# Kernel tuning notes

Hardware: AMD Instinct MI355X
Metric: run time of the kernel (lower is better)

## Reference

```python
import jax, jax.numpy as jnp
import numpy as np

B, LQ, LK, H = 16, 8192, 128, 128  # note LK == H is required by the final matmul
SCALE = float(np.sqrt(H))


def setup_inputs() -> dict:
    key = jax.random.key(0)
    k1, k2, k3, k4, k5, k6 = jax.random.split(key, 6)
    x1 = jax.random.normal(k1, (B, LQ, H), dtype=jnp.float32)
    x2 = jax.random.normal(k2, (B, LK, H), dtype=jnp.float32)
    x3 = jax.random.randint(k3, (B, LQ, LK), 0, 2).astype(bool)
    bound = 1.0 / np.sqrt(H)  # torch Linear default init
    wq = jax.random.uniform(k4, (H, H), minval=-bound, maxval=bound, dtype=jnp.float32)
    wk = jax.random.uniform(k5, (H, H), minval=-bound, maxval=bound, dtype=jnp.float32)
    wv = jax.random.uniform(k6, (H, H), minval=-bound, maxval=bound, dtype=jnp.float32)
    return {"x1": x1, "x2": x2, "x3": x3, "wq": wq, "wk": wk, "wv": wv}


def reference(x1, x2, x3, wq, wk, wv):
    q = x1 @ wq.T                                   # (B, Lq, H)
    k = x2 @ wk.T                                   # (B, Lk, H)
    qk = jnp.einsum('bqh,bkh->bqk', q, k) / SCALE   # (B, Lq, Lk)
    qk = jnp.where(x3, -jnp.inf, qk)                # masked_fill_ where mask is True
    attn_weight = jax.nn.softmax(qk, axis=-1)       # softmax over Lk
    v = x2 @ wv.T                                   # (B, Lk, H)
    # v @ attn_weight^T: contracts v's H axis with attn_weight's Lk axis (H == Lk)
    attn = jnp.matmul(v, jnp.swapaxes(attn_weight, -2, -1))  # (B, Lk, Lq)
    return attn
```

## Files before the change

kernel.cpp:

```cpp
#include <hip/hip_runtime.h>
#include <hip/hip_bf16.h>
#include <stdint.h>

typedef __bf16 bf16_t;
typedef __bf16 bf16x8 __attribute__((ext_vector_type(8)));
typedef float  f32x4  __attribute__((ext_vector_type(4)));
typedef float  f32x16 __attribute__((ext_vector_type(16)));
typedef unsigned int uint;
typedef uint uintx4 __attribute__((ext_vector_type(4)));

#define MFMA16(a,b,c) __builtin_amdgcn_mfma_f32_16x16x32_bf16((a),(b),(c),0,0,0)
#define MFMA32(a,b,c) __builtin_amdgcn_mfma_f32_32x32x16_bf16((a),(b),(c),0,0,0)

constexpr int NB = 16;
constexpr int LQ = 8192;
constexpr int LK = 128;
constexpr int H  = 128;

constexpr float C1 = 1.4426950408889634f / 11.313708498984761f;

constexpr size_t WS_FLAG = 0;
constexpr size_t WS_MV   = 1024;

__device__ __forceinline__ unsigned swz(unsigned row, unsigned byte) {
  return row * 256u + (byte ^ ((row & 15u) << 4));
}

__device__ __forceinline__ bf16x8 cvt_frag(const float* p) {
  f32x4 u0 = *(const f32x4*)p;
  f32x4 u1 = *(const f32x4*)(p + 4);
  bf16x8 v;
  #pragma unroll
  for (int e = 0; e < 4; ++e) { v[e] = (bf16_t)u0[e]; v[e + 4] = (bf16_t)u1[e]; }
  return v;
}

__device__ __forceinline__ f32x16 zero16() {
  f32x16 z;
  #pragma unroll
  for (int i = 0; i < 16; ++i) z[i] = 0.f;
  return z;
}

__device__ __forceinline__ uint pkbf(float a, float b) {
  uint d;
  asm("v_cvt_pk_bf16_f32 %0, %1, %2" : "=v"(d) : "v"(a), "v"(b));
  return d;
}

__device__ __forceinline__ void gl16(const void* g, void* l) {
  __builtin_amdgcn_global_load_lds(
      (const __attribute__((address_space(1))) uint32_t*)g,
      (__attribute__((address_space(3))) uint32_t*)l, 16, 0, 0);
}

__global__ __launch_bounds__(512) void prep_kernel(
    const float* __restrict__ x2, const float* __restrict__ wq,
    const float* __restrict__ wk, const float* __restrict__ wv,
    const unsigned* __restrict__ x3w, uint8_t* __restrict__ ws)
{
  __shared__ uint8_t sP[131072];
  __shared__ int sF32, sBig;
  const int tid = threadIdx.x;
  const int b = blockIdx.x >> 1, which = blockIdx.x & 1;
  const int l = tid & 63, w = tid >> 6, q31 = l & 31, hi2 = l >> 5;
  uint8_t* sOut = sP + 98304;

  if (which == 0) {
    if (blockIdx.x == 0) {
      if (tid == 0) { sF32 = 0; sBig = 0; }
      __syncthreads();
      int f = 0, g = 0;
      #pragma unroll
      for (int j = 0; j < 4; ++j) {
        unsigned v = x3w[tid * 4 + j];
        if (v == 0x3f800000u) f = 1;
        else if (v > 1u) g = 1;
      }
      if (f) sF32 = 1;
      if (g) sBig = 1;
      __syncthreads();
      if (tid == 0) *(int*)(ws + WS_FLAG) = (sF32 == 0 && sBig == 1) ? 1 : 0;
    }

    {
      const int row = tid >> 2, c0 = (tid & 3) * 32;
      #pragma unroll
      for (int wh = 0; wh < 2; ++wh) {
        const float* W = wh ? wk : wq;
        uint8_t* dst = sP + wh * 32768;
        const float* s = W + row * H + c0;
        #pragma unroll
        for (int j = 0; j < 32; ++j)
          *(bf16_t*)(dst + swz(c0 + j, row * 2)) = (bf16_t)s[j];
      }
    }
    __syncthreads();

    {
      const int lo = l & 15, hi = l >> 4;
      bf16x8 a4[4];
      #pragma unroll
      for (int kk = 0; kk < 4; ++kk)
        a4[kk] = *(const bf16x8*)(sP + swz(16 * w + lo, kk * 64 + hi * 16));
      bf16_t* W2T = (bf16_t*)(sP + 65536);
      #pragma unroll
      for (int t = 0; t < 8; ++t) {
        f32x4 c = {0.f, 0.f, 0.f, 0.f};
        #pragma unroll
        for (int kk = 0; kk < 4; ++kk)
          c = MFMA16(a4[kk], *(const bf16x8*)(sP + 32768 + swz(16 * t + lo, kk * 64 + hi * 16)), c);
        #pragma unroll
        for (int r = 0; r < 4; ++r)
          W2T[(16 * w + hi * 4 + r) * H + 16 * t + lo] = (bf16_t)c[r];
      }
    }
    __syncthreads();

    if (w < 4) {
      const int wb = w;
      bf16x8 axf[8];
      const float* x2r = x2 + ((size_t)b * LK + 32 * wb + q31) * H;
      #pragma unroll
      for (int kt = 0; kt < 8; ++kt)
        axf[kt] = cvt_frag(x2r + kt * 16 + 8 * hi2);
      const bf16_t* W2Tl = (const bf16_t*)(sP + 65536);
      #pragma unroll
      for (int nt = 0; nt < 4; ++nt) {
        f32x16 c = zero16();
        #pragma unroll
        for (int kt = 0; kt < 8; ++kt)
          c = MFMA32(axf[kt],
                     *(const bf16x8*)(W2Tl + (size_t)(nt * 32 + q31) * H + kt * 16 + 8 * hi2), c);
        #pragma unroll
        for (int r = 0; r < 16; ++r)
          *(bf16_t*)(sOut + swz(32 * wb + (r & 3) + 8 * (r >> 2) + 4 * hi2,
                                (nt * 32 + q31) * 2)) = (bf16_t)c[r];
      }
    }
  } else {
    if (w < 4) {
      const int wb = w;
      bf16x8 axf[8];
      const float* x2r = x2 + ((size_t)b * LK + 32 * wb + q31) * H;
      #pragma unroll
      for (int kt = 0; kt < 8; ++kt)
        axf[kt] = cvt_frag(x2r + kt * 16 + 8 * hi2);
      #pragma unroll
      for (int nt = 0; nt < 4; ++nt) {
        f32x16 c = zero16();
        #pragma unroll
        for (int kt = 0; kt < 8; ++kt)
          c = MFMA32(axf[kt],
                     cvt_frag(wv + (size_t)(nt * 32 + q31) * H + kt * 16 + 8 * hi2), c);
        #pragma unroll
        for (int r = 0; r < 16; ++r)
          *(bf16_t*)(sOut + swz(32 * wb + (r & 3) + 8 * (r >> 2) + 4 * hi2,
                                (nt * 32 + q31) * 2)) = (bf16_t)c[r];
      }
    }
  }
  __syncthreads();

  {
    const uint4* src = (const uint4*)sOut;
    uint4* dst = (uint4*)(ws + WS_MV + (size_t)b * 65536 + (size_t)which * 32768);
    #pragma unroll
    for (int j = 0; j < 4; ++j)
      dst[tid + j * 512] = src[tid + j * 512];
  }
}


#define CONV_S_PB(XR, MU, QROW)                                                \
  {                                                                            \
    bf16x8 xbf[8];                                                             \
    _Pragma("unroll")                                                          \
    for (int kt = 0; kt < 8; ++kt) {                                           \
      _Pragma("unroll")                                                        \
      for (int e = 0; e < 4; ++e) {                                            \
        xbf[kt][e]     = (bf16_t)XR[2 * kt][e];                                \
        xbf[kt][e + 4] = (bf16_t)XR[2 * kt + 1][e];                            \
      }                                                                        \
    }                                                                          \
    const uint* mrowW = (const uint*)x3 + (QROW) * LK;                         \
    _Pragma("unroll")                                                          \
    for (int half = 0; half < 2; ++half) {                                     \
      const int jt0 = half * 2, jt1 = half * 2 + 1;                            \
      f32x16 s0 = zero16(), s1 = zero16();                                     \
      __builtin_amdgcn_s_setprio(1);                                           \
      _Pragma("unroll")                                                        \
      for (int kt = 0; kt < 8; ++kt) {                                         \
        s0 = MFMA32(*(const bf16x8*)(sM + swz(jt0 * 32 + q31, kt * 32 + hi2 * 16)), \
                    xbf[kt], s0);                                              \
        s1 = MFMA32(*(const bf16x8*)(sM + swz(jt1 * 32 + q31, kt * 32 + hi2 * 16)), \
                    xbf[kt], s1);                                              \
      }                                                                        \
      __builtin_amdgcn_s_setprio(0);                                           \
      _Pragma("unroll")                                                        \
      for (int jj = 0; jj < 2; ++jj) {                                         \
        f32x16& sj = jj ? s1 : s0;                                             \
        const int jt = half * 2 + jj;                                          \
        _Pragma("unroll")                                                      \
        for (int rg = 0; rg < 4; ++rg) {                                       \
          uint m0, m1, m2, m3;                                                 \
          if (byteMode) {                                                      \
            uint u = MU[jt * 4 + rg];                                          \
            m0 = u & 0xffu; m1 = (u >> 8) & 0xffu;                             \
            m2 = (u >> 16) & 0xffu; m3 = u >> 24;                              \
          } else {                                                             \
            uint4 mw = *(const uint4*)(mrowW + jt * 32 + 8 * rg + 4 * hi2);    \
            m0 = mw.x; m1 = mw.y; m2 = mw.z; m3 = mw.w;                        \
          }                                                                    \
          float p0 = __builtin_amdgcn_exp2f(sj[rg * 4 + 0] * C1);              \
          float p1 = __builtin_amdgcn_exp2f(sj[rg * 4 + 1] * C1);              \
          float p2 = __builtin_amdgcn_exp2f(sj[rg * 4 + 2] * C1);              \
          float p3 = __builtin_amdgcn_exp2f(sj[rg * 4 + 3] * C1);              \
          sj[rg * 4 + 0] = m0 ? 0.f : p0;                                      \
          sj[rg * 4 + 1] = m1 ? 0.f : p1;                                      \
          sj[rg * 4 + 2] = m2 ? 0.f : p2;                                      \
          sj[rg * 4 + 3] = m3 ? 0.f : p3;                                      \
        }                                                                      \
        _Pragma("unroll")                                                      \
        for (int h = 0; h < 2; ++h) {                                          \
          uint A = pkbf(sj[h * 8 + 0], sj[h * 8 + 1]);                         \
          uint C = pkbf(sj[h * 8 + 2], sj[h * 8 + 3]);                         \
          uint B = pkbf(sj[h * 8 + 4], sj[h * 8 + 5]);                         \
          uint D = pkbf(sj[h * 8 + 6], sj[h * 8 + 7]);                         \
          asm("v_permlane32_swap_b32 %0, %1" : "+v"(A), "+v"(B));              \
          asm("v_permlane32_swap_b32 %0, %1" : "+v"(C), "+v"(D));              \
          uintx4 t2; t2.x = A; t2.y = C; t2.z = B; t2.w = D;                   \
          pb[jt * 2 + h] = __builtin_bit_cast(bf16x8, t2);                     \
        }                                                                      \
      }                                                                        \
    }                                                                          \
  }

#define O_STORE(Q0W)                                                           \
  {                                                                            \
    f32x16 dacc = zero16();                                                    \
    {                                                                          \
      f32x16 o0 = zero16(), o1 = zero16();                                     \
      __builtin_amdgcn_s_setprio(1);                                           \
      _Pragma("unroll")                                                        \
      for (int kt = 0; kt < 8; ++kt) {                                         \
        dacc = MFMA32(ones1, pb[kt], dacc);                                    \
        o0 = MFMA32(*(const bf16x8*)(sV + swz(0 * 32 + q31, kt * 32 + hi2 * 16)), pb[kt], o0); \
        o1 = MFMA32(*(const bf16x8*)(sV + swz(1 * 32 + q31, kt * 32 + hi2 * 16)), pb[kt], o1); \
      }                                                                        \
      __builtin_amdgcn_s_setprio(0);                                           \
      const float inv = 1.0f / dacc[0];                                        \
      _Pragma("unroll")                                                        \
      for (int r = 0; r < 16; ++r) {                                           \
        const int ibase = (r & 3) + 8 * (r >> 2) + 4 * hi2;                    \
        __builtin_nontemporal_store(o0[r] * inv,                               \
            &out[((size_t)b * LK + ibase) * LQ + (Q0W) + q31]);                \
        __builtin_nontemporal_store(o1[r] * inv,                               \
            &out[((size_t)b * LK + 32 + ibase) * LQ + (Q0W) + q31]);           \
      }                                                                        \
      f32x16 o2 = zero16(), o3 = zero16();                                     \
      __builtin_amdgcn_s_setprio(1);                                           \
      _Pragma("unroll")                                                        \
      for (int kt = 0; kt < 8; ++kt) {                                         \
        o2 = MFMA32(*(const bf16x8*)(sV + swz(2 * 32 + q31, kt * 32 + hi2 * 16)), pb[kt], o2); \
        o3 = MFMA32(*(const bf16x8*)(sV + swz(3 * 32 + q31, kt * 32 + hi2 * 16)), pb[kt], o3); \
      }                                                                        \
      __builtin_amdgcn_s_setprio(0);                                           \
      _Pragma("unroll")                                                        \
      for (int r = 0; r < 16; ++r) {                                           \
        const int ibase = (r & 3) + 8 * (r >> 2) + 4 * hi2;                    \
        __builtin_nontemporal_store(o2[r] * inv,                               \
            &out[((size_t)b * LK + 64 + ibase) * LQ + (Q0W) + q31]);           \
        __builtin_nontemporal_store(o3[r] * inv,                               \
            &out[((size_t)b * LK + 96 + ibase) * LQ + (Q0W) + q31]);           \
      }                                                                        \
    }                                                                          \
  }

__global__ __launch_bounds__(256, 2) void attn_kernel(
    const float* __restrict__ x1, const void* __restrict__ x3,
    const uint8_t* __restrict__ ws, float* __restrict__ out)
{
  __shared__ uint8_t sm[65536];
  uint8_t* sM = sm;
  uint8_t* sV = sm + 32768;

  const int tid = threadIdx.x, blk = blockIdx.x;
  const int xcd = blk & 7;
  const int t   = blk >> 3;
  const int b   = ((t & 1) << 3) | xcd;
  const int qc  = (t >> 1) * 256;
  const int l = tid & 63, w4 = tid >> 6;
  const int q31 = l & 31, hi2 = l >> 5;
  const int byteMode = *(const int*)(ws + WS_FLAG);

  const int q0w0 = qc + w4 * 64;
  const int q0w1 = q0w0 + 32;
  const size_t qrow0 = (size_t)b * LQ + q0w0 + q31;
  const size_t qrow1 = qrow0 + 32;

  {
    const uint8_t* g = ws + WS_MV + (size_t)b * 65536;
    #pragma unroll
    for (int j = 0; j < 16; ++j)
      gl16(g + tid * 16 + j * 4096, sm + tid * 16 + j * 4096);
  }

  f32x4 xr0[16];
  uint mu0[16];
  {
    const float* xp = x1 + qrow0 * H;
    #pragma unroll
    for (int kt = 0; kt < 8; ++kt) {
      xr0[2 * kt]     = *(const f32x4*)(xp + kt * 16 + 8 * hi2);
      xr0[2 * kt + 1] = *(const f32x4*)(xp + kt * 16 + 8 * hi2 + 4);
    }
    if (byteMode) {
      const uint8_t* mp = (const uint8_t*)x3 + qrow0 * LK;
      #pragma unroll
      for (int jt = 0; jt < 4; ++jt)
        #pragma unroll
        for (int rg = 0; rg < 4; ++rg)
          mu0[jt * 4 + rg] = *(const uint*)(mp + jt * 32 + 8 * rg + 4 * hi2);
    }
  }
  __syncthreads();

  bf16x8 ones1;
  #pragma unroll
  for (int e = 0; e < 8; ++e) ones1[e] = (bf16_t)1.f;

  bf16x8 pb[8];

  CONV_S_PB(xr0, mu0, qrow0)

  f32x4 xr1[16];
  uint mu1[16];
  {
    const float* xp = x1 + qrow1 * H;
    #pragma unroll
    for (int kt = 0; kt < 8; ++kt) {
      xr1[2 * kt]     = *(const f32x4*)(xp + kt * 16 + 8 * hi2);
      xr1[2 * kt + 1] = *(const f32x4*)(xp + kt * 16 + 8 * hi2 + 4);
    }
    if (byteMode) {
      const uint8_t* mp = (const uint8_t*)x3 + qrow1 * LK;
      #pragma unroll
      for (int jt = 0; jt < 4; ++jt)
        #pragma unroll
        for (int rg = 0; rg < 4; ++rg)
          mu1[jt * 4 + rg] = *(const uint*)(mp + jt * 32 + 8 * rg + 4 * hi2);
    }
  }

  O_STORE(q0w0)

  CONV_S_PB(xr1, mu1, qrow1)
  O_STORE(q0w1)
}

extern "C" void kernel_launch(void* const* d_in, const int* in_sizes, int n_in,
                              void* d_out, int out_size, void* d_ws, size_t ws_size,
                              hipStream_t stream) {
  const float* x1 = (const float*)d_in[0];
  const float* x2 = (const float*)d_in[1];
  const void*  x3 = d_in[2];
  const float* wq = (const float*)d_in[3];
  const float* wk = (const float*)d_in[4];
  const float* wv = (const float*)d_in[5];
  uint8_t* ws = (uint8_t*)d_ws;
  float* out = (float*)d_out;

  prep_kernel<<<2 * NB, 512, 0, stream>>>(x2, wq, wk, wv, (const unsigned*)x3, ws);
  attn_kernel<<<NB * (LQ / 256), 256, 0, stream>>>(x1, x3, ws, out);
}
```

Before: 47.40 us.

## Pack boolean mask into bitmask in prep kernel before attention

Adds 512 extra blocks to the prep kernel that read the mask (byte or word format) and compress each 128-entry row into 16 bytes with wave ballots, stored in the workspace. The attention kernel then loads one 16-byte vector per row and tests bits, instead of reading 128 bytes or 512 bytes of mask per row. This cuts mask bandwidth and load instructions in the main kernel. The cost is an extra full pass over the mask in the prep launch, which serializes before attention, and the prep blocks' 128KB LDS allocation may limit how many of them run at once.

```diff
diff --git a/kernel.cpp b/kernel.cpp
--- a/kernel.cpp
+++ b/kernel.cpp
@@ -19,8 +19,8 @@
 
 constexpr float C1 = 1.4426950408889634f / 11.313708498984761f;
 
-constexpr size_t WS_FLAG = 0;
-constexpr size_t WS_MV   = 1024;
+constexpr size_t WS_MV = 1024;
+constexpr size_t WS_BM = WS_MV + (size_t)NB * 65536;
 
 __device__ __forceinline__ unsigned swz(unsigned row, unsigned byte) {
   return row * 256u + (byte ^ ((row & 15u) << 4));
@@ -57,32 +57,58 @@
 __global__ __launch_bounds__(512) void prep_kernel(
     const float* __restrict__ x2, const float* __restrict__ wq,
     const float* __restrict__ wk, const float* __restrict__ wv,
-    const unsigned* __restrict__ x3w, uint8_t* __restrict__ ws)
+    const void* __restrict__ x3, uint8_t* __restrict__ ws)
 {
   __shared__ uint8_t sP[131072];
   __shared__ int sF32, sBig;
   const int tid = threadIdx.x;
-  const int b = blockIdx.x >> 1, which = blockIdx.x & 1;
   const int l = tid & 63, w = tid >> 6, q31 = l & 31, hi2 = l >> 5;
-  uint8_t* sOut = sP + 98304;
-
-  if (which == 0) {
-    if (blockIdx.x == 0) {
-      if (tid == 0) { sF32 = 0; sBig = 0; }
-      __syncthreads();
+
+  if (blockIdx.x >= 32) {
+    const int pb = blockIdx.x - 32;
+    if (tid == 0) { sF32 = 0; sBig = 0; }
+    __syncthreads();
+    {
+      const uint* x3w = (const uint*)x3;
       int f = 0, g = 0;
       #pragma unroll
       for (int j = 0; j < 4; ++j) {
-        unsigned v = x3w[tid * 4 + j];
+        uint v = x3w[tid * 4 + j];
         if (v == 0x3f800000u) f = 1;
         else if (v > 1u) g = 1;
       }
       if (f) sF32 = 1;
       if (g) sBig = 1;
-      __syncthreads();
-      if (tid == 0) *(int*)(ws + WS_FLAG) = (sF32 == 0 && sBig == 1) ? 1 : 0;
-    }
-
+    }
+    __syncthreads();
+    const int byteMode = (sF32 == 0 && sBig == 1) ? 1 : 0;
+
+    uint8_t* bm = ws + WS_BM;
+    #pragma unroll 4
+    for (int rr = 0; rr < 32; ++rr) {
+      const size_t row = (size_t)pb * 256 + w * 32 + rr;
+      unsigned long long b0, b1;
+      if (byteMode) {
+        const uint8_t* rp = (const uint8_t*)x3 + row * 128;
+        b0 = __ballot(rp[l] != 0);
+        b1 = __ballot(rp[64 + l] != 0);
+      } else {
+        const uint* rp = (const uint*)x3 + row * 128;
+        b0 = __ballot(rp[l] != 0);
+        b1 = __ballot(rp[64 + l] != 0);
+      }
+      if (l == 0) {
+        *(unsigned long long*)(bm + row * 16)     = b0;
+        *(unsigned long long*)(bm + row * 16 + 8) = b1;
+      }
+    }
+    return;
+  }
+
+  const int b = blockIdx.x >> 1, which = blockIdx.x & 1;
+  uint8_t* sOut = sP + 98304;
+
+  if (which == 0) {
     {
       const int row = tid >> 2, c0 = (tid & 3) * 32;
       #pragma unroll
@@ -172,7 +198,7 @@
 }
 
 
-#define CONV_S_PB(XR, MU, QROW)                                                \
+#define CONV_S_PB(XR, MB)                                                      \
   {                                                                            \
     bf16x8 xbf[8];                                                             \
     _Pragma("unroll")                                                          \
@@ -183,7 +209,6 @@
         xbf[kt][e + 4] = (bf16_t)XR[2 * kt + 1][e];                            \
       }                                                                        \
     }                                                                          \
-    const uint* mrowW = (const uint*)x3 + (QROW) * LK;                         \
     _Pragma("unroll")                                                          \
     for (int half = 0; half < 2; ++half) {                                     \
       const int jt0 = half * 2, jt1 = half * 2 + 1;                            \
@@ -203,23 +228,15 @@
         const int jt = half * 2 + jj;                                          \
         _Pragma("unroll")                                                      \
         for (int rg = 0; rg < 4; ++rg) {                                       \
-          uint m0, m1, m2, m3;                                                 \
-          if (byteMode) {                                                      \
-            uint u = MU[jt * 4 + rg];                                          \
-            m0 = u & 0xffu; m1 = (u >> 8) & 0xffu;                             \
-            m2 = (u >> 16) & 0xffu; m3 = u >> 24;                              \
-          } else {                                                             \
-            uint4 mw = *(const uint4*)(mrowW + jt * 32 + 8 * rg + 4 * hi2);    \
-            m0 = mw.x; m1 = mw.y; m2 = mw.z; m3 = mw.w;                        \
-          }                                                                    \
+          const uint mw = MB[jt] >> (8 * rg + 4 * hi2);                        \
           float p0 = __builtin_amdgcn_exp2f(sj[rg * 4 + 0] * C1);              \
           float p1 = __builtin_amdgcn_exp2f(sj[rg * 4 + 1] * C1);              \
           float p2 = __builtin_amdgcn_exp2f(sj[rg * 4 + 2] * C1);              \
           float p3 = __builtin_amdgcn_exp2f(sj[rg * 4 + 3] * C1);              \
-          sj[rg * 4 + 0] = m0 ? 0.f : p0;                                      \
-          sj[rg * 4 + 1] = m1 ? 0.f : p1;                                      \
-          sj[rg * 4 + 2] = m2 ? 0.f : p2;                                      \
-          sj[rg * 4 + 3] = m3 ? 0.f : p3;                                      \
+          sj[rg * 4 + 0] = (mw & 1u) ? 0.f : p0;                               \
+          sj[rg * 4 + 1] = (mw & 2u) ? 0.f : p1;                               \
+          sj[rg * 4 + 2] = (mw & 4u) ? 0.f : p2;                               \
+          sj[rg * 4 + 3] = (mw & 8u) ? 0.f : p3;                               \
         }                                                                      \
         _Pragma("unroll")                                                      \
         for (int h = 0; h < 2; ++h) {                                          \
@@ -278,8 +295,8 @@
   }
 
 __global__ __launch_bounds__(256, 2) void attn_kernel(
-    const float* __restrict__ x1, const void* __restrict__ x3,
-    const uint8_t* __restrict__ ws, float* __restrict__ out)
+    const float* __restrict__ x1, const uint8_t* __restrict__ ws,
+    float* __restrict__ out)
 {
   __shared__ uint8_t sm[65536];
   uint8_t* sM = sm;
@@ -292,12 +309,13 @@
   const int qc  = (t >> 1) * 256;
   const int l = tid & 63, w4 = tid >> 6;
   const int q31 = l & 31, hi2 = l >> 5;
-  const int byteMode = *(const int*)(ws + WS_FLAG);
 
   const int q0w0 = qc + w4 * 64;
   const int q0w1 = q0w0 + 32;
   const size_t qrow0 = (size_t)b * LQ + q0w0 + q31;
   const size_t qrow1 = qrow0 + 32;
+
+  const uint8_t* bm = ws + WS_BM;
 
   {
     const uint8_t* g = ws + WS_MV + (size_t)b * 65536;
@@ -307,7 +325,7 @@
   }
 
   f32x4 xr0[16];
-  uint mu0[16];
+  uintx4 mb0;
   {
     const float* xp = x1 + qrow0 * H;
     #pragma unroll
@@ -315,14 +333,7 @@
       xr0[2 * kt]     = *(const f32x4*)(xp + kt * 16 + 8 * hi2);
       xr0[2 * kt + 1] = *(const f32x4*)(xp + kt * 16 + 8 * hi2 + 4);
     }
-    if (byteMode) {
-      const uint8_t* mp = (const uint8_t*)x3 + qrow0 * LK;
-      #pragma unroll
-      for (int jt = 0; jt < 4; ++jt)
-        #pragma unroll
-        for (int rg = 0; rg < 4; ++rg)
-          mu0[jt * 4 + rg] = *(const uint*)(mp + jt * 32 + 8 * rg + 4 * hi2);
-    }
+    mb0 = *(const uintx4*)(bm + qrow0 * 16);
   }
   __syncthreads();
 
@@ -332,10 +343,10 @@
 
   bf16x8 pb[8];
 
-  CONV_S_PB(xr0, mu0, qrow0)
+  CONV_S_PB(xr0, mb0)
 
   f32x4 xr1[16];
-  uint mu1[16];
+  uintx4 mb1;
   {
     const float* xp = x1 + qrow1 * H;
     #pragma unroll
@@ -343,19 +354,12 @@
       xr1[2 * kt]     = *(const f32x4*)(xp + kt * 16 + 8 * hi2);
       xr1[2 * kt + 1] = *(const f32x4*)(xp + kt * 16 + 8 * hi2 + 4);
     }
-    if (byteMode) {
-      const uint8_t* mp = (const uint8_t*)x3 + qrow1 * LK;
-      #pragma unroll
-      for (int jt = 0; jt < 4; ++jt)
-        #pragma unroll
-        for (int rg = 0; rg < 4; ++rg)
-          mu1[jt * 4 + rg] = *(const uint*)(mp + jt * 32 + 8 * rg + 4 * hi2);
-    }
+    mb1 = *(const uintx4*)(bm + qrow1 * 16);
   }
 
   O_STORE(q0w0)
 
-  CONV_S_PB(xr1, mu1, qrow1)
+  CONV_S_PB(xr1, mb1)
   O_STORE(q0w1)
 }
 
@@ -371,6 +375,6 @@
   uint8_t* ws = (uint8_t*)d_ws;
   float* out = (float*)d_out;
 
-  prep_kernel<<<2 * NB, 512, 0, stream>>>(x2, wq, wk, wv, (const unsigned*)x3, ws);
-  attn_kernel<<<NB * (LQ / 256), 256, 0, stream>>>(x1, x3, ws, out);
-}
+  prep_kernel<<<32 + 512, 512, 0, stream>>>(x2, wq, wk, wv, x3, ws);
+  attn_kernel<<<NB * (LQ / 256), 256, 0, stream>>>(x1, ws, out);
+}
```

Result: slower. 63.41 us (+33.8%).
